# Kernel tuning notes

Measured on AMD Instinct MI355X. Metric: run time of the kernel, lower is better.

## Reference

```python
import jax, jax.numpy as jnp
import numpy as np

N_N = 100000
N_E = 1600000
IN_DIM = 128
OUT_DIM = 128


def setup_inputs() -> dict:
    key = jax.random.key(0)
    k1, k2, k3, k4 = jax.random.split(key, 4)
    feats_n = jax.random.normal(k1, (N_N, IN_DIM), dtype=jnp.float32)
    # hs: guarantee every node appears at least once as a row (head) so degree > 0,
    # matching well-posed inputs for D**(-1/2) in the original module.
    hs = jnp.concatenate([
        jnp.arange(N_N, dtype=jnp.int64),
        jax.random.randint(k2, (N_E - N_N,), 0, N_N, dtype=jnp.int64),
    ])
    ts = jax.random.randint(k3, (N_E,), 0, N_N, dtype=jnp.int64)
    edges = jnp.stack([hs, ts], axis=0)  # [2, N_e]
    # Linear weight: normal(0,1) scaled by 1/sqrt(out_dim), no bias.
    weight = jax.random.normal(k4, (OUT_DIM, IN_DIM), dtype=jnp.float32) / np.sqrt(OUT_DIM)
    return {"feats_n": feats_n, "edges": edges, "weight": weight}


def reference(feats_n, edges, weight):
    hs, ts = edges[0], edges[1]
    n = feats_n.shape[0]
    # Degree = row-sum of adjacency (rows indexed by hs)
    deg = jax.ops.segment_sum(jnp.ones_like(hs, dtype=feats_n.dtype), hs, num_segments=n)
    sqrt_d_inv = deg ** (-0.5)  # [N_n]
    scaled = sqrt_d_inv[:, None] * feats_n  # [N_n, d]
    # SpMM: out[h] = sum over edges (h, t) of scaled[t]
    agg = jax.ops.segment_sum(scaled[ts], hs, num_segments=n)  # [N_n, d]
    msg = sqrt_d_inv[:, None] * agg
    out = msg @ weight.T  # Linear, no bias
    return jax.nn.relu(out)
```

## Files before the change

kernel.cpp:

```cpp
#include <hip/hip_runtime.h>

#define IN_DIM 128
#define CAP 64
#define NODE_SHIFT 8
#define BIN_NODES 256
#define NB_MAX 512
#define BCAP 5120
#define BINCAP_E 10240
#define CHUNK 4096
#define SMEM_BYTES 32768

typedef __attribute__((ext_vector_type(8))) short bf16x8;
typedef __attribute__((ext_vector_type(4))) float f32x4;
typedef __attribute__((ext_vector_type(2))) float f32x2;

struct PtLds { int hist[NB_MAX]; int base[NB_MAX]; unsigned int sp[CHUNK]; };
struct BsLds { unsigned int sp[BCAP]; int lcur[BIN_NODES]; int sbase[BIN_NODES];
               int wsum[4]; };

__device__ __forceinline__ unsigned short f2bf(float f) {
    unsigned int u = __float_as_uint(f);
    u += 0x7FFFu + ((u >> 16) & 1u);
    return (unsigned short)(u >> 16);
}

__device__ __forceinline__ void dev_partition(char* smem, int c, const int* __restrict__ edges,
                                              int n_e, int nbins,
                                              unsigned int* __restrict__ pairs,
                                              int* __restrict__ bincur) {
    PtLds* pt = (PtLds*)smem;
    int tid = threadIdx.x;
    int e0 = c * CHUNK;
    int nloc = n_e - e0;
    if (nloc > CHUNK) nloc = CHUNK;
    int nloc4 = nloc >> 2;
    const int* hsrc = edges + e0;
    const int* tsrc = edges + n_e + e0;
    for (int i = tid; i < nbins; i += 256) pt->hist[i] = 0;
    __syncthreads();
    for (int j = tid; j < nloc4; j += 256) {
        int4 hv = ((const int4*)hsrc)[j];
        int4 tv = ((const int4*)tsrc)[j];
        pt->sp[4 * j + 0] = ((unsigned int)(hv.x & 255) << 17) | (unsigned int)tv.x;
        pt->sp[4 * j + 1] = ((unsigned int)(hv.y & 255) << 17) | (unsigned int)tv.y;
        pt->sp[4 * j + 2] = ((unsigned int)(hv.z & 255) << 17) | (unsigned int)tv.z;
        pt->sp[4 * j + 3] = ((unsigned int)(hv.w & 255) << 17) | (unsigned int)tv.w;
        atomicAdd(&pt->hist[hv.x >> NODE_SHIFT], 1);
        atomicAdd(&pt->hist[hv.y >> NODE_SHIFT], 1);
        atomicAdd(&pt->hist[hv.z >> NODE_SHIFT], 1);
        atomicAdd(&pt->hist[hv.w >> NODE_SHIFT], 1);
    }
    for (int i = (nloc4 << 2) + tid; i < nloc; i += 256) {
        int h = hsrc[i];
        pt->sp[i] = ((unsigned int)(h & 255) << 17) | (unsigned int)tsrc[i];
        atomicAdd(&pt->hist[h >> NODE_SHIFT], 1);
    }
    __syncthreads();
    for (int b = tid; b < nbins; b += 256) {
        int cc = pt->hist[b];
        pt->base[b] = cc ? atomicAdd(&bincur[b], cc) : 0;
        pt->hist[b] = 0;
    }
    __syncthreads();
    for (int j = tid; j < nloc4; j += 256) {
        int4 hv = ((const int4*)hsrc)[j];
        int bi[4] = {hv.x >> NODE_SHIFT, hv.y >> NODE_SHIFT,
                     hv.z >> NODE_SHIFT, hv.w >> NODE_SHIFT};
        #pragma unroll
        for (int k = 0; k < 4; ++k) {
            int b = bi[k];
            int pos = atomicAdd(&pt->hist[b], 1);
            int g = pt->base[b] + pos;
            if (g < BCAP) pairs[(size_t)b * BCAP + g] = pt->sp[4 * j + k];
        }
    }
    for (int i = (nloc4 << 2) + tid; i < nloc; i += 256) {
        int b = hsrc[i] >> NODE_SHIFT;
        int pos = atomicAdd(&pt->hist[b], 1);
        int g = pt->base[b] + pos;
        if (g < BCAP) pairs[(size_t)b * BCAP + g] = pt->sp[i];
    }
    __syncthreads();
}

__device__ __forceinline__ void dev_binscatter(char* smem, int b,
                                               const unsigned int* __restrict__ pairs,
                                               const int* __restrict__ bincur,
                                               int* __restrict__ bucket,
                                               int2* __restrict__ rowinfo,
                                               float* __restrict__ rsd,
                                               float* __restrict__ rowscale, int n_n) {
    BsLds* bs = (BsLds*)smem;
    int tid = threadIdx.x;
    bs->lcur[tid] = 0;
    __syncthreads();
    int n = bincur[b];
    if (n > BCAP) n = BCAP;
    const unsigned int* pp = pairs + (size_t)b * BCAP;
    for (int i = tid; i < n; i += 256) {
        unsigned int p = pp[i];
        bs->sp[i] = p;
        atomicAdd(&bs->lcur[p >> 17], 1);
    }
    __syncthreads();
    int draw = bs->lcur[tid];
    int dcap = draw < CAP ? draw : CAP;
    int v = (dcap + 15) & ~15;
    int lane = tid & 63, w = tid >> 6;
    int x = v;
    #pragma unroll
    for (int off = 1; off < 64; off <<= 1) {
        int y = __shfl_up(x, off);
        if (lane >= off) x += y;
    }
    if (lane == 63) bs->wsum[w] = x;
    __syncthreads();
    int wo = 0;
    for (int k = 0; k < w; ++k) wo += bs->wsum[k];
    int mybase = wo + x - v;
    bs->sbase[tid] = mybase;
    bs->lcur[tid] = 0;
    __syncthreads();
    int gbase = b * BINCAP_E;
    for (int i = tid; i < n; i += 256) {
        unsigned int p = bs->sp[i];
        int li = p >> 17;
        int t = p & 0x1FFFF;
        int pos = atomicAdd(&bs->lcur[li], 1);
        if (pos < CAP) {
            int idx = bs->sbase[li] + pos;
            if (idx < BINCAP_E) bucket[gbase + idx] = t;
        }
    }
    __syncthreads();
    int h = (b << NODE_SHIFT) + tid;
    if (h < n_n) {
        for (int s = dcap; s < v; ++s) {
            int idx = mybase + s;
            if (idx < BINCAP_E) bucket[gbase + idx] = n_n;
        }
        rowinfo[h] = make_int2(gbase + mybase, dcap);
        rsd[h] = draw > 0 ? rsqrtf((float)draw) : 0.0f;
    } else if (h == n_n) {
        rsd[n_n] = 0.0f;
        rowscale[n_n] = 0.0f;
    }
    __syncthreads();
}

__device__ __forceinline__ void dev_wconv(char* smem, const float* __restrict__ W) {
    bf16x8* wl = (bf16x8*)smem;
    int tid = threadIdx.x;
    #pragma unroll
    for (int k = 0; k < 8; ++k) {
        int gi = tid + k * 256;
        int n = gi >> 4, g = gi & 15;
        const float* wp = W + n * IN_DIM + g * 8;
        float4 a = *(const float4*)wp;
        float4 b2 = *(const float4*)(wp + 4);
        bf16x8 v;
        v[0] = (short)f2bf(a.x); v[1] = (short)f2bf(a.y);
        v[2] = (short)f2bf(a.z); v[3] = (short)f2bf(a.w);
        v[4] = (short)f2bf(b2.x); v[5] = (short)f2bf(b2.y);
        v[6] = (short)f2bf(b2.z); v[7] = (short)f2bf(b2.w);
        wl[n * 16 + (g ^ (n & 7))] = v;
    }
    __syncthreads();
}

__device__ __forceinline__ void dev_gemm(char* smem, int mb, const float* __restrict__ X,
                                         unsigned char* __restrict__ Y8,
                                         float* __restrict__ rowscale, int M) {
    const bf16x8* wl = (const bf16x8*)smem;
    int tid = threadIdx.x;
    int slab = mb * 4 + (tid >> 6);
    int m0 = slab * 16;
    if (m0 >= M) return;
    int l = tid & 63;
    int lm = l & 15, lk = l >> 4;
    int row = m0 + lm;
    int rowc = row < M ? row : M - 1;
    bf16x8 xf[4];
    const float* xbase = X + (size_t)rowc * IN_DIM + lk * 8;
    #pragma unroll
    for (int ks = 0; ks < 4; ++ks) {
        float4 a = *(const float4*)(xbase + ks * 32);
        float4 b2 = *(const float4*)(xbase + ks * 32 + 4);
        bf16x8 v;
        v[0] = (short)f2bf(a.x); v[1] = (short)f2bf(a.y);
        v[2] = (short)f2bf(a.z); v[3] = (short)f2bf(a.w);
        v[4] = (short)f2bf(b2.x); v[5] = (short)f2bf(b2.y);
        v[6] = (short)f2bf(b2.z); v[7] = (short)f2bf(b2.w);
        xf[ks] = v;
    }
    f32x4 acc[8];
    #pragma unroll
    for (int nt = 0; nt < 8; ++nt) {
        acc[nt][0] = 0.f; acc[nt][1] = 0.f; acc[nt][2] = 0.f; acc[nt][3] = 0.f;
        #pragma unroll
        for (int ks = 0; ks < 4; ++ks) {
            int nn = nt * 16 + lm;
            int g = ks * 4 + lk;
            bf16x8 wf = wl[nn * 16 + (g ^ (nn & 7))];
            acc[nt] = __builtin_amdgcn_mfma_f32_16x16x32_bf16(wf, xf[ks], acc[nt], 0, 0, 0);
        }
    }
    float mx = 0.f;
    #pragma unroll
    for (int nt = 0; nt < 8; ++nt) {
        mx = fmaxf(mx, fmaxf(fmaxf(fabsf(acc[nt][0]), fabsf(acc[nt][1])),
                             fmaxf(fabsf(acc[nt][2]), fabsf(acc[nt][3]))));
    }
    mx = fmaxf(mx, __shfl_xor(mx, 16));
    mx = fmaxf(mx, __shfl_xor(mx, 32));
    float inv = mx > 0.f ? 127.0f / mx : 0.f;
    if (row >= M) return;
    if (lk == 0) rowscale[row] = mx * (1.0f / 127.0f);
    unsigned char* yb = Y8 + (size_t)row * IN_DIM;
    #pragma unroll
    for (int nt = 0; nt < 8; ++nt) {
        unsigned int wd = 0;
        #pragma unroll
        for (int r = 0; r < 4; ++r) {
            int q = (int)rintf(acc[nt][r] * inv);
            q = q < -127 ? -127 : (q > 127 ? 127 : q);
            wd |= (unsigned int)(q + 128) << (8 * r);
        }
        *(unsigned int*)(yb + nt * 16 + lk * 4) = wd;
    }
}

__global__ __launch_bounds__(256, 4) void k_phaseA(const int* __restrict__ edges, int n_e,
                                                   int nbins, int npart, int mbA, int split,
                                                   unsigned int* __restrict__ pairs,
                                                   int* __restrict__ bincur,
                                                   const float* __restrict__ X,
                                                   const float* __restrict__ W,
                                                   unsigned char* __restrict__ Y8,
                                                   float* __restrict__ rowscale, int n_n) {
    extern __shared__ char smem[];
    int bid = blockIdx.x, NB = gridDim.x;
    if (bid < split) {
        for (int c = bid; c < npart; c += split)
            dev_partition(smem, c, edges, n_e, nbins, pairs, bincur);
    } else {
        dev_wconv(smem, W);
        for (int mb = bid - split; mb < mbA; mb += NB - split)
            dev_gemm(smem, mb, X, Y8, rowscale, n_n);
    }
}

__global__ __launch_bounds__(256, 4) void k_phaseB(int nbins, int mbA, int nmf, int split,
                                                   const unsigned int* __restrict__ pairs,
                                                   const int* __restrict__ bincur,
                                                   int* __restrict__ bucket,
                                                   int2* __restrict__ rowinfo,
                                                   float* __restrict__ rsd,
                                                   const float* __restrict__ X,
                                                   const float* __restrict__ W,
                                                   unsigned char* __restrict__ Y8,
                                                   float* __restrict__ rowscale, int n_n) {
    extern __shared__ char smem[];
    int bid = blockIdx.x, NB = gridDim.x;
    if (bid < split) {
        for (int b = bid; b < nbins; b += split)
            dev_binscatter(smem, b, pairs, bincur, bucket, rowinfo, rsd, rowscale, n_n);
    } else {
        dev_wconv(smem, W);
        for (int mb = mbA + (bid - split); mb < nmf; mb += NB - split)
            dev_gemm(smem, mb, X, Y8, rowscale, n_n);
    }
}

__global__ __launch_bounds__(256) void k_agg(const uint2* __restrict__ Y8v,
                                             const int* __restrict__ bucket,
                                             const int2* __restrict__ rowinfo,
                                             const float* __restrict__ rsd,
                                             const float* __restrict__ rowscale,
                                             float* __restrict__ out, int n_n) {
    int gw = (int)((blockIdx.x * 256u + threadIdx.x) >> 6);
    int lane = threadIdx.x & 63;
    if (gw >= n_n) return;
    int2 ri = rowinfo[gw];
    int d = ri.y;
    int nb = (d + 15) >> 4;
    const uint4* bk4 = (const uint4*)(bucket + ri.x);
    int grp = lane >> 4, a = lane & 15;
    f32x2 a0 = {0.f, 0.f}, a1 = {0.f, 0.f}, a2 = {0.f, 0.f}, a3 = {0.f, 0.f};
    float S = 0.f;

    #define CVT0(U, F) asm("v_cvt_f32_ubyte0 %0, %1" : "=v"(F) : "v"(U));
    #define CVT1(U, F) asm("v_cvt_f32_ubyte1 %0, %1" : "=v"(F) : "v"(U));
    #define CVT2(U, F) asm("v_cvt_f32_ubyte2 %0, %1" : "=v"(F) : "v"(U));
    #define CVT3(U, F) asm("v_cvt_f32_ubyte3 %0, %1" : "=v"(F) : "v"(U));

    uint4 tv = bk4[grp];
    for (int b = 0; b < nb; ++b) {
        int bn = (b + 1 < nb) ? b + 1 : b;
        uint4 tvn = bk4[bn * 4 + grp];
        float c0 = rsd[tv.x] * rowscale[tv.x];
        float c1 = rsd[tv.y] * rowscale[tv.y];
        float c2 = rsd[tv.z] * rowscale[tv.z];
        float c3 = rsd[tv.w] * rowscale[tv.w];
        uint2 v0 = Y8v[(size_t)tv.x * 16 + a];
        uint2 v1 = Y8v[(size_t)tv.y * 16 + a];
        uint2 v2 = Y8v[(size_t)tv.z * 16 + a];
        uint2 v3 = Y8v[(size_t)tv.w * 16 + a];
        #define ACCUM(V, C)                                                   \
        {                                                                     \
            S += (C);                                                         \
            f32x2 sv; sv[0] = (C); sv[1] = (C);                               \
            f32x2 x;                                                          \
            CVT0((V).x, x[0]) CVT1((V).x, x[1])                               \
            asm("v_pk_fma_f32 %0, %1, %2, %0" : "+v"(a0) : "v"(x), "v"(sv));  \
            CVT2((V).x, x[0]) CVT3((V).x, x[1])                               \
            asm("v_pk_fma_f32 %0, %1, %2, %0" : "+v"(a1) : "v"(x), "v"(sv));  \
            CVT0((V).y, x[0]) CVT1((V).y, x[1])                               \
            asm("v_pk_fma_f32 %0, %1, %2, %0" : "+v"(a2) : "v"(x), "v"(sv));  \
            CVT2((V).y, x[0]) CVT3((V).y, x[1])                               \
            asm("v_pk_fma_f32 %0, %1, %2, %0" : "+v"(a3) : "v"(x), "v"(sv));  \
        }
        ACCUM(v0, c0) ACCUM(v1, c1) ACCUM(v2, c2) ACCUM(v3, c3)
        #undef ACCUM
        tv = tvn;
    }
    #define MERGE(A)                                                          \
    {                                                                         \
        A[0] += __shfl_xor(A[0], 16); A[1] += __shfl_xor(A[1], 16);           \
        A[0] += __shfl_xor(A[0], 32); A[1] += __shfl_xor(A[1], 32);           \
    }
    MERGE(a0) MERGE(a1) MERGE(a2) MERGE(a3)
    #undef MERGE
    S += __shfl_xor(S, 16);
    S += __shfl_xor(S, 32);
    if (lane < 16) {
        float adj = 128.0f * S;
        float s = rsd[gw];
        float4 o0 = make_float4(fmaxf((a0[0] - adj) * s, 0.f), fmaxf((a0[1] - adj) * s, 0.f),
                                fmaxf((a1[0] - adj) * s, 0.f), fmaxf((a1[1] - adj) * s, 0.f));
        float4 o1 = make_float4(fmaxf((a2[0] - adj) * s, 0.f), fmaxf((a2[1] - adj) * s, 0.f),
                                fmaxf((a3[0] - adj) * s, 0.f), fmaxf((a3[1] - adj) * s, 0.f));
        float4* op = (float4*)(out + (size_t)gw * IN_DIM + a * 8);
        op[0] = o0;
        op[1] = o1;
    }
    #undef CVT0
    #undef CVT1
    #undef CVT2
    #undef CVT3
}

extern "C" void kernel_launch(void* const* d_in, const int* in_sizes, int n_in,
                              void* d_out, int out_size, void* d_ws, size_t ws_size,
                              hipStream_t stream) {
    const float* X = (const float*)d_in[0];
    const int* edges = (const int*)d_in[1];
    const float* W = (const float*)d_in[2];
    int n_n = in_sizes[0] / IN_DIM;
    int n_e = in_sizes[1] / 2;
    int nbins = (n_n + BIN_NODES - 1) >> NODE_SHIFT;

    char* ws = (char*)d_ws;
    size_t o = 0;
    auto take = [&](size_t bytes) -> char* {
        char* p = ws + o;
        o += (bytes + 511) & ~(size_t)511;
        return p;
    };
    float* rsd = (float*)take((size_t)(n_n + 1) * 4);
    float* rowscale = (float*)take((size_t)(n_n + 1) * 4);
    int2* rowinfo = (int2*)take((size_t)n_n * 8);
    int* bucket = (int*)take((size_t)nbins * BINCAP_E * 4);
    unsigned char* Y8 = (unsigned char*)take((size_t)(n_n + 1) * IN_DIM);
    unsigned int* pairs = (unsigned int*)take((size_t)nbins * BCAP * 4);
    int* bincur = (int*)take((size_t)nbins * 4);

    int nslab = (n_n + 15) / 16;
    int nmf = (nslab + 3) / 4;
    int mbA = (nmf * 5) / 6;
    int npart = (n_e + CHUNK - 1) / CHUNK;
    int split = nbins;

    hipMemsetAsync(bincur, 0, (size_t)nbins * 4, stream);
    k_phaseA<<<1024, 256, SMEM_BYTES, stream>>>(edges, n_e, nbins, npart, mbA, split,
                                                pairs, bincur, X, W, Y8, rowscale, n_n);
    k_phaseB<<<1024, 256, SMEM_BYTES, stream>>>(nbins, mbA, nmf, split, pairs, bincur,
                                                bucket, rowinfo, rsd, X, W, Y8, rowscale, n_n);
    k_agg<<<(n_n + 3) / 4, 256, 0, stream>>>((const uint2*)Y8, bucket, rowinfo, rsd,
                                             rowscale, (float*)d_out, n_n);
}
```

Baseline: 110.4 us.

## Move all GEMM to phase A, precombine row scales, use byte offsets in agg

The GEMM work is no longer split between phase A and phase B. Phase A now computes every GEMM tile, and phase B only does the bin scatter, launched with one block per bin. Phase B also writes a combined per-node scale (rsqrt degree times quantization scale), so the aggregation kernel does one gather per neighbour instead of two. The aggregation kernel uses 32-bit byte-offset addressing to cut 64-bit address arithmetic. The trade-off is that phase A gets more work on its critical path, and there is an extra small array to write.

```diff
diff --git a/kernel.cpp b/kernel.cpp
--- a/kernel.cpp
+++ b/kernel.cpp
@@ -89,7 +89,8 @@
                                                int* __restrict__ bucket,
                                                int2* __restrict__ rowinfo,
                                                float* __restrict__ rsd,
-                                               float* __restrict__ rowscale, int n_n) {
+                                               const float* __restrict__ rowscale,
+                                               float* __restrict__ comb, int n_n) {
     BsLds* bs = (BsLds*)smem;
     int tid = threadIdx.x;
     bs->lcur[tid] = 0;
@@ -140,10 +141,12 @@
             if (idx < BINCAP_E) bucket[gbase + idx] = n_n;
         }
         rowinfo[h] = make_int2(gbase + mybase, dcap);
-        rsd[h] = draw > 0 ? rsqrtf((float)draw) : 0.0f;
+        float r = draw > 0 ? rsqrtf((float)draw) : 0.0f;
+        rsd[h] = r;
+        comb[h] = r * rowscale[h];
     } else if (h == n_n) {
         rsd[n_n] = 0.0f;
-        rowscale[n_n] = 0.0f;
+        comb[n_n] = 0.0f;
     }
     __syncthreads();
 }
@@ -231,7 +234,7 @@
 }
 
 __global__ __launch_bounds__(256, 4) void k_phaseA(const int* __restrict__ edges, int n_e,
-                                                   int nbins, int npart, int mbA, int split,
+                                                   int nbins, int npart, int nmf, int split,
                                                    unsigned int* __restrict__ pairs,
                                                    int* __restrict__ bincur,
                                                    const float* __restrict__ X,
@@ -245,47 +248,40 @@
             dev_partition(smem, c, edges, n_e, nbins, pairs, bincur);
     } else {
         dev_wconv(smem, W);
-        for (int mb = bid - split; mb < mbA; mb += NB - split)
+        for (int mb = bid - split; mb < nmf; mb += NB - split)
             dev_gemm(smem, mb, X, Y8, rowscale, n_n);
     }
 }
 
-__global__ __launch_bounds__(256, 4) void k_phaseB(int nbins, int mbA, int nmf, int split,
+__global__ __launch_bounds__(256, 4) void k_phaseB(int nbins,
                                                    const unsigned int* __restrict__ pairs,
                                                    const int* __restrict__ bincur,
                                                    int* __restrict__ bucket,
                                                    int2* __restrict__ rowinfo,
                                                    float* __restrict__ rsd,
-                                                   const float* __restrict__ X,
-                                                   const float* __restrict__ W,
-                                                   unsigned char* __restrict__ Y8,
-                                                   float* __restrict__ rowscale, int n_n) {
+                                                   const float* __restrict__ rowscale,
+                                                   float* __restrict__ comb, int n_n) {
     extern __shared__ char smem[];
-    int bid = blockIdx.x, NB = gridDim.x;
-    if (bid < split) {
-        for (int b = bid; b < nbins; b += split)
-            dev_binscatter(smem, b, pairs, bincur, bucket, rowinfo, rsd, rowscale, n_n);
-    } else {
-        dev_wconv(smem, W);
-        for (int mb = mbA + (bid - split); mb < nmf; mb += NB - split)
-            dev_gemm(smem, mb, X, Y8, rowscale, n_n);
-    }
-}
-
-__global__ __launch_bounds__(256) void k_agg(const uint2* __restrict__ Y8v,
-                                             const int* __restrict__ bucket,
+    dev_binscatter(smem, blockIdx.x, pairs, bincur, bucket, rowinfo, rsd,
+                   rowscale, comb, n_n);
+}
+
+__global__ __launch_bounds__(256) void k_agg(const char* __restrict__ Y8b,
+                                             const char* __restrict__ bucketb,
                                              const int2* __restrict__ rowinfo,
                                              const float* __restrict__ rsd,
-                                             const float* __restrict__ rowscale,
+                                             const char* __restrict__ combb,
                                              float* __restrict__ out, int n_n) {
     int gw = (int)((blockIdx.x * 256u + threadIdx.x) >> 6);
     int lane = threadIdx.x & 63;
     if (gw >= n_n) return;
     int2 ri = rowinfo[gw];
+    float sg = rsd[gw];
     int d = ri.y;
     int nb = (d + 15) >> 4;
-    const uint4* bk4 = (const uint4*)(bucket + ri.x);
     int grp = lane >> 4, a = lane & 15;
+    unsigned int bko = ((unsigned int)ri.x << 2) + ((unsigned int)grp << 4);
+    unsigned int ao8 = (unsigned int)a << 3;
     f32x2 a0 = {0.f, 0.f}, a1 = {0.f, 0.f}, a2 = {0.f, 0.f}, a3 = {0.f, 0.f};
     float S = 0.f;
 
@@ -294,18 +290,18 @@
     #define CVT2(U, F) asm("v_cvt_f32_ubyte2 %0, %1" : "=v"(F) : "v"(U));
     #define CVT3(U, F) asm("v_cvt_f32_ubyte3 %0, %1" : "=v"(F) : "v"(U));
 
-    uint4 tv = bk4[grp];
+    uint4 tv = *(const uint4*)(bucketb + bko);
     for (int b = 0; b < nb; ++b) {
-        int bn = (b + 1 < nb) ? b + 1 : b;
-        uint4 tvn = bk4[bn * 4 + grp];
-        float c0 = rsd[tv.x] * rowscale[tv.x];
-        float c1 = rsd[tv.y] * rowscale[tv.y];
-        float c2 = rsd[tv.z] * rowscale[tv.z];
-        float c3 = rsd[tv.w] * rowscale[tv.w];
-        uint2 v0 = Y8v[(size_t)tv.x * 16 + a];
-        uint2 v1 = Y8v[(size_t)tv.y * 16 + a];
-        uint2 v2 = Y8v[(size_t)tv.z * 16 + a];
-        uint2 v3 = Y8v[(size_t)tv.w * 16 + a];
+        unsigned int bn = (unsigned int)((b + 1 < nb) ? b + 1 : b);
+        uint4 tvn = *(const uint4*)(bucketb + bko + (bn << 6));
+        float c0 = *(const float*)(combb + (tv.x << 2));
+        float c1 = *(const float*)(combb + (tv.y << 2));
+        float c2 = *(const float*)(combb + (tv.z << 2));
+        float c3 = *(const float*)(combb + (tv.w << 2));
+        uint2 v0 = *(const uint2*)(Y8b + (tv.x << 7) + ao8);
+        uint2 v1 = *(const uint2*)(Y8b + (tv.y << 7) + ao8);
+        uint2 v2 = *(const uint2*)(Y8b + (tv.z << 7) + ao8);
+        uint2 v3 = *(const uint2*)(Y8b + (tv.w << 7) + ao8);
         #define ACCUM(V, C)                                                   \
         {                                                                     \
             S += (C);                                                         \
@@ -335,11 +331,10 @@
     S += __shfl_xor(S, 32);
     if (lane < 16) {
         float adj = 128.0f * S;
-        float s = rsd[gw];
-        float4 o0 = make_float4(fmaxf((a0[0] - adj) * s, 0.f), fmaxf((a0[1] - adj) * s, 0.f),
-                                fmaxf((a1[0] - adj) * s, 0.f), fmaxf((a1[1] - adj) * s, 0.f));
-        float4 o1 = make_float4(fmaxf((a2[0] - adj) * s, 0.f), fmaxf((a2[1] - adj) * s, 0.f),
-                                fmaxf((a3[0] - adj) * s, 0.f), fmaxf((a3[1] - adj) * s, 0.f));
+        float4 o0 = make_float4(fmaxf((a0[0] - adj) * sg, 0.f), fmaxf((a0[1] - adj) * sg, 0.f),
+                                fmaxf((a1[0] - adj) * sg, 0.f), fmaxf((a1[1] - adj) * sg, 0.f));
+        float4 o1 = make_float4(fmaxf((a2[0] - adj) * sg, 0.f), fmaxf((a2[1] - adj) * sg, 0.f),
+                                fmaxf((a3[0] - adj) * sg, 0.f), fmaxf((a3[1] - adj) * sg, 0.f));
         float4* op = (float4*)(out + (size_t)gw * IN_DIM + a * 8);
         op[0] = o0;
         op[1] = o1;
@@ -369,6 +364,7 @@
     };
     float* rsd = (float*)take((size_t)(n_n + 1) * 4);
     float* rowscale = (float*)take((size_t)(n_n + 1) * 4);
+    float* comb = (float*)take((size_t)(n_n + 1) * 4);
     int2* rowinfo = (int2*)take((size_t)n_n * 8);
     int* bucket = (int*)take((size_t)nbins * BINCAP_E * 4);
     unsigned char* Y8 = (unsigned char*)take((size_t)(n_n + 1) * IN_DIM);
@@ -377,15 +373,15 @@
 
     int nslab = (n_n + 15) / 16;
     int nmf = (nslab + 3) / 4;
-    int mbA = (nmf * 5) / 6;
     int npart = (n_e + CHUNK - 1) / CHUNK;
     int split = nbins;
 
     hipMemsetAsync(bincur, 0, (size_t)nbins * 4, stream);
-    k_phaseA<<<1024, 256, SMEM_BYTES, stream>>>(edges, n_e, nbins, npart, mbA, split,
+    k_phaseA<<<1024, 256, SMEM_BYTES, stream>>>(edges, n_e, nbins, npart, nmf, split,
                                                 pairs, bincur, X, W, Y8, rowscale, n_n);
-    k_phaseB<<<1024, 256, SMEM_BYTES, stream>>>(nbins, mbA, nmf, split, pairs, bincur,
-                                                bucket, rowinfo, rsd, X, W, Y8, rowscale, n_n);
-    k_agg<<<(n_n + 3) / 4, 256, 0, stream>>>((const uint2*)Y8, bucket, rowinfo, rsd,
-                                             rowscale, (float*)d_out, n_n);
-}
+    k_phaseB<<<nbins, 256, SMEM_BYTES, stream>>>(nbins, pairs, bincur, bucket, rowinfo,
+                                                 rsd, rowscale, comb, n_n);
+    k_agg<<<(n_n + 3) / 4, 256, 0, stream>>>((const char*)Y8, (const char*)bucket,
+                                             rowinfo, rsd, (const char*)comb,
+                                             (float*)d_out, n_n);
+}
```

Measured after the change: 106.0 us. -4.0%, faster.
